# Performance work log

Hardware: AMD Instinct MI355X
Metric: run time of the kernel (lower is better)

## Reference

```python
import jax, jax.numpy as jnp
import numpy as np

DEPTH, HEADS, DIM_HEAD = 6, 12, 64
DIM, MLP, FEAT = 768, 3072, 1000
B, N = 32, 196
EPS = 1e-5


def layernorm(x, g, b):
    m = jnp.mean(x, axis=-1, keepdims=True)
    v = jnp.var(x, axis=-1, keepdims=True)
    return (x - m) * jax.lax.rsqrt(v + EPS) * g + b


def setup_inputs() -> dict:
    key = jax.random.key(0)
    ks = jax.random.split(key, 8)
    s = 0.02
    return {
        "x": jax.random.normal(ks[0], (B, N, DIM), jnp.float32),
        "cls_token": jax.random.normal(ks[1], (1, 1, DIM), jnp.float32),
        "ln1_g": jnp.ones((DEPTH, DIM), jnp.float32),
        "ln1_b": jnp.zeros((DEPTH, DIM), jnp.float32),
        "w_qkv": jax.random.normal(ks[2], (DEPTH, DIM, 3 * HEADS * DIM_HEAD), jnp.float32) * s,
        "reattn_w": jax.random.normal(ks[3], (DEPTH, HEADS, HEADS), jnp.float32),
        "reattn_g": jnp.ones((DEPTH, HEADS), jnp.float32),
        "reattn_b": jnp.zeros((DEPTH, HEADS), jnp.float32),
        "w_out": jax.random.normal(ks[4], (DEPTH, HEADS * DIM_HEAD, DIM), jnp.float32) * s,
        "b_out": jnp.zeros((DEPTH, DIM), jnp.float32),
        "ln2_g": jnp.ones((DEPTH, DIM), jnp.float32),
        "ln2_b": jnp.zeros((DEPTH, DIM), jnp.float32),
        "w1": jax.random.normal(ks[5], (DEPTH, DIM, MLP), jnp.float32) * s,
        "b1": jnp.zeros((DEPTH, MLP), jnp.float32),
        "w2": jax.random.normal(ks[6], (DEPTH, MLP, DIM), jnp.float32) * s,
        "b2": jnp.zeros((DEPTH, DIM), jnp.float32),
        "lnf_g": jnp.ones((DIM,), jnp.float32),
        "lnf_b": jnp.zeros((DIM,), jnp.float32),
        "w_head": jax.random.normal(ks[7], (DIM, FEAT), jnp.float32) * s,
        "b_head": jnp.zeros((FEAT,), jnp.float32),
    }


def _forward(x, cls_token, ln1_g, ln1_b, w_qkv, reattn_w, reattn_g, reattn_b,
             w_out, b_out, ln2_g, ln2_b, w1, b1, w2, b2, lnf_g, lnf_b, w_head, b_head):
    b = x.shape[0]
    cls = jnp.broadcast_to(cls_token, (b, 1, DIM))
    x = jnp.concatenate([cls, x], axis=1)  # (B, N+1, DIM)
    n = x.shape[1]
    scale = DIM_HEAD ** -0.5
    for l in range(DEPTH):
        h = layernorm(x, ln1_g[l], ln1_b[l])
        qkv = h @ w_qkv[l]                       # (B, n, 3*H*Dh)
        qkv = qkv.reshape(b, n, 3, HEADS, DIM_HEAD)
        q, k, v = (qkv[:, :, i].transpose(0, 2, 1, 3) for i in range(3))  # b h n d
        dots = jnp.einsum('bhid,bhjd->bhij', q, k) * scale
        attn = jax.nn.softmax(dots, axis=-1)
        attn = jnp.einsum('bhij,hg->bgij', attn, reattn_w[l])
        # per-head LayerNorm: normalize over head axis (axis=1)
        m = jnp.mean(attn, axis=1, keepdims=True)
        var = jnp.var(attn, axis=1, keepdims=True)
        attn = (attn - m) * jax.lax.rsqrt(var + EPS)
        attn = attn * reattn_g[l][None, :, None, None] + reattn_b[l][None, :, None, None]
        out = jnp.einsum('bhij,bhjd->bhid', attn, v)
        out = out.transpose(0, 2, 1, 3).reshape(b, n, HEADS * DIM_HEAD)
        x = x + out @ w_out[l] + b_out[l]
        h = layernorm(x, ln2_g[l], ln2_b[l])
        h = jax.nn.gelu(h @ w1[l] + b1[l], approximate=False)
        x = x + h @ w2[l] + b2[l]
    pooled = x[:, 0]  # cls pool
    return layernorm(pooled, lnf_g, lnf_b) @ w_head + b_head


def reference(x, cls_token, ln1_g, ln1_b, w_qkv, reattn_w, reattn_g, reattn_b,
              w_out, b_out, ln2_g, ln2_b, w1, b1, w2, b2, lnf_g, lnf_b, w_head, b_head):
    return _forward(x, cls_token, ln1_g, ln1_b, w_qkv, reattn_w, reattn_g, reattn_b,
                    w_out, b_out, ln2_g, ln2_b, w1, b1, w2, b2, lnf_g, lnf_b, w_head, b_head)
```

## Files before the change

kernel.cpp:

```cpp
#include <hip/hip_runtime.h>
#include <cstdint>

typedef __bf16 bf16_t;
typedef __bf16 bf16x8 __attribute__((ext_vector_type(8)));
typedef float  f32x4  __attribute__((ext_vector_type(4)));
typedef unsigned int u32;

#define DEPTH 6
#define HEADS 12
#define DH    64
#define DIM   768
#define MLPD  3072
#define FEAT  1000
#define BATCH 32
#define SEQ   197
#define NP    224
#define TOK   (BATCH*SEQ)

__device__ __forceinline__ f32x4 zero4() {
    f32x4 z; z[0] = 0.f; z[1] = 0.f; z[2] = 0.f; z[3] = 0.f; return z;
}

__device__ __forceinline__ f32x4 mfma16(bf16x8 a, bf16x8 b, f32x4 c) {
    return __builtin_amdgcn_mfma_f32_16x16x32_bf16(a, b, c, 0, 0, 0);
}

typedef const __attribute__((address_space(1))) u32* gas_ptr;
typedef __attribute__((address_space(3))) u32*       las_ptr;
__device__ __forceinline__ void gload16(const bf16_t* g, bf16_t* l) {
    __builtin_amdgcn_global_load_lds((gas_ptr)g, (las_ptr)l, 16, 0, 0);
}

__global__ __launch_bounds__(256) void concat_k(const float* __restrict__ x,
                                                const float* __restrict__ cls,
                                                float* __restrict__ xbuf) {
    int idx = blockIdx.x * 256 + threadIdx.x;
    int col = idx % DIM;
    int row = idx / DIM;
    int b = row / SEQ, p = row % SEQ;
    xbuf[idx] = (p == 0) ? cls[col] : x[(b * 196 + p - 1) * DIM + col];
}

__global__ __launch_bounds__(256) void tcvt_k(const float* __restrict__ W,
                                              bf16_t* __restrict__ Wt,
                                              int K, int N) {
    __shared__ float t[32][33];
    int n0 = blockIdx.x * 32, k0 = blockIdx.y * 32;
    int c = threadIdx.x & 31, r = threadIdx.x >> 5;
#pragma unroll
    for (int i = 0; i < 4; i++) {
        int k = k0 + r + i * 8, n = n0 + c;
        t[r + i * 8][c] = (n < N) ? W[k * N + n] : 0.f;
    }
    __syncthreads();
#pragma unroll
    for (int i = 0; i < 4; i++) {
        int n = n0 + r + i * 8, k = k0 + c;
        if (n < N) Wt[n * K + k] = (bf16_t)t[c][r + i * 8];
    }
}

__global__ __launch_bounds__(256) void tcvtall_k(const float* __restrict__ wq,
                                                 const float* __restrict__ wo,
                                                 const float* __restrict__ w1p,
                                                 const float* __restrict__ w2p,
                                                 bf16_t* __restrict__ wt) {
    int id = blockIdx.x;
    const float* W; int K, N, ntx, rid; long doff;
    if (id < 1728)      { W = wq;  K = 768;  N = 2304; doff = 0;       ntx = 72; rid = id; }
    else if (id < 2304) { W = wo;  K = 768;  N = 768;  doff = 1769472; ntx = 24; rid = id - 1728; }
    else if (id < 4608) { W = w1p; K = 768;  N = 3072; doff = 2359296; ntx = 96; rid = id - 2304; }
    else                { W = w2p; K = 3072; N = 768;  doff = 4718592; ntx = 24; rid = id - 4608; }
    int n0 = (rid % ntx) * 32, k0 = (rid / ntx) * 32;
    __shared__ float t[32][33];
    int c = threadIdx.x & 31, r = threadIdx.x >> 5;
#pragma unroll
    for (int i = 0; i < 4; i++)
        t[r + i * 8][c] = W[(long)(k0 + r + i * 8) * N + n0 + c];
    __syncthreads();
#pragma unroll
    for (int i = 0; i < 4; i++)
        wt[doff + (long)(n0 + r + i * 8) * K + k0 + c] = (bf16_t)t[c][r + i * 8];
}

__global__ __launch_bounds__(256) void ln_k(const float* __restrict__ x, long row_stride,
                                            const float* __restrict__ g,
                                            const float* __restrict__ b,
                                            bf16_t* __restrict__ out) {
    int row = blockIdx.x;
    const float* xr = x + (long)row * row_stride;
    int t = threadIdx.x;
    float v0 = xr[t], v1 = xr[t + 256], v2 = xr[t + 512];
    float s  = v0 + v1 + v2;
    float sq = v0 * v0 + v1 * v1 + v2 * v2;
#pragma unroll
    for (int o = 1; o < 64; o <<= 1) { s += __shfl_xor(s, o); sq += __shfl_xor(sq, o); }
    __shared__ float ss[4], sqs[4];
    int w = t >> 6;
    if ((t & 63) == 0) { ss[w] = s; sqs[w] = sq; }
    __syncthreads();
    s  = ss[0] + ss[1] + ss[2] + ss[3];
    sq = sqs[0] + sqs[1] + sqs[2] + sqs[3];
    float m  = s * (1.f / 768.f);
    float rs = rsqrtf(sq * (1.f / 768.f) - m * m + 1e-5f);
    bf16_t* orow = out + (long)row * DIM;
    orow[t]       = (bf16_t)((v0 - m) * rs * g[t]       + b[t]);
    orow[t + 256] = (bf16_t)((v1 - m) * rs * g[t + 256] + b[t + 256]);
    orow[t + 512] = (bf16_t)((v2 - m) * rs * g[t + 512] + b[t + 512]);
}

template <int MODE>
__global__ __launch_bounds__(512) void gemm_k(const bf16_t* __restrict__ A,
                                              const bf16_t* __restrict__ Bt,
                                              const float* __restrict__ bias,
                                              float* __restrict__ Cf,
                                              bf16_t* __restrict__ Cb,
                                              int M, int N, int Kstride, int Klen) {
    __shared__ bf16_t sA[2][128][32];
    __shared__ bf16_t sB[2][256][32];
    int tid = threadIdx.x;
    int bm = blockIdx.x * 128, bn = blockIdx.y * 256;
    long koff = (long)blockIdx.z * Klen;
    int wave = tid >> 6, lane = tid & 63;
    int wm = (wave >> 2) * 64, wn = (wave & 3) * 64;
    int la = lane & 15, lb = lane >> 4;

    int trow = tid >> 2, colE = (tid & 3) * 8;
    int rowA = bm + trow; if (rowA > M - 1) rowA = M - 1;
    int rowB0 = bn + trow, rowB1 = bn + 128 + trow;

    f32x4 acc[4][4];
#pragma unroll
    for (int m = 0; m < 4; m++)
#pragma unroll
        for (int n = 0; n < 4; n++) acc[m][n] = zero4();

    auto stage = [&](int buf, long k0) {
        gload16(A  + (long)rowA  * Kstride + k0 + colE, &sA[buf][0][0] + wave * 512);
        gload16(Bt + (long)rowB0 * Kstride + k0 + colE, &sB[buf][0][0] + wave * 512);
        gload16(Bt + (long)rowB1 * Kstride + k0 + colE, &sB[buf][0][0] + 4096 + wave * 512);
    };

    int nt = Klen >> 5;
    stage(0, koff);
    __syncthreads();
    for (int t = 0; t < nt; t++) {
        int cur = t & 1;
        if (t + 1 < nt) stage(cur ^ 1, koff + ((long)(t + 1) << 5));
        bf16x8 af[4], bfr[4];
#pragma unroll
        for (int m = 0; m < 4; m++) af[m]  = *(const bf16x8*)&sA[cur][wm + m * 16 + la][lb * 8];
#pragma unroll
        for (int n = 0; n < 4; n++) bfr[n] = *(const bf16x8*)&sB[cur][wn + n * 16 + la][lb * 8];
#pragma unroll
        for (int m = 0; m < 4; m++)
#pragma unroll
            for (int n = 0; n < 4; n++)
                acc[m][n] = mfma16(af[m], bfr[n], acc[m][n]);
        __syncthreads();
    }

    long kout = (long)blockIdx.z * M * (long)N;
#pragma unroll
    for (int m = 0; m < 4; m++) {
#pragma unroll
        for (int n = 0; n < 4; n++) {
            int ib = bm + wm + m * 16 + lb * 4;
            int jb = bn + wn + n * 16 + la;
            float bv = (MODE == 1 || MODE == 2) ? bias[jb] : 0.f;
#pragma unroll
            for (int r = 0; r < 4; r++) {
                int i = ib + r;
                if (i >= M) continue;
                float v = acc[m][n][r];
                if (MODE == 0) {
                    Cb[(long)i * N + jb] = (bf16_t)v;
                } else if (MODE == 1) {
                    Cf[(long)i * N + jb] += v + bv;
                } else if (MODE == 2) {
                    float u = v + bv;
                    Cb[(long)i * N + jb] = (bf16_t)(0.5f * u * (1.f + erff(u * 0.70710678118f)));
                } else {
                    Cf[kout + (long)i * N + jb] = v;
                }
            }
        }
    }
}

__global__ __launch_bounds__(256) void redk_k(float* __restrict__ xbuf,
                                              const float* __restrict__ part,
                                              const float* __restrict__ bias) {
    const long total = (long)TOK * DIM;
    for (long idx = blockIdx.x * 256 + threadIdx.x; idx < total; idx += (long)gridDim.x * 256) {
        int col = (int)(idx % DIM);
        xbuf[idx] += part[idx] + part[idx + total] + bias[col];
    }
}

__global__ __launch_bounds__(256) void gemm_h(const bf16_t* __restrict__ A,
                                              const bf16_t* __restrict__ Bt,
                                              const float* __restrict__ bias,
                                              float* __restrict__ Cf,
                                              int M, int N, int K) {
    __shared__ bf16_t sA[2][128][32];
    __shared__ bf16_t sB[2][128][32];
    int tid = threadIdx.x;
    int bm = blockIdx.x * 128, bn = blockIdx.y * 128;
    int wave = tid >> 6, lane = tid & 63;
    int wm = (wave >> 1) * 64, wn = (wave & 1) * 64;
    int la = lane & 15, lb = lane >> 4;
    int rowA[2], rowB[2], colE[2];
#pragma unroll
    for (int q = 0; q < 2; q++) {
        int li = (wave * 2 + q) * 64 + lane;
        int row = li >> 2;
        colE[q] = (li & 3) * 8;
        int ar = bm + row; if (ar > M - 1) ar = M - 1;
        int br = bn + row; if (br > N - 1) br = N - 1;
        rowA[q] = ar; rowB[q] = br;
    }
    f32x4 acc[4][4];
#pragma unroll
    for (int m = 0; m < 4; m++)
#pragma unroll
        for (int n = 0; n < 4; n++) acc[m][n] = zero4();
    int nt = K >> 5;
#pragma unroll
    for (int q = 0; q < 2; q++) {
        gload16(A  + (long)rowA[q] * K + colE[q], &sA[0][0][0] + (wave * 2 + q) * 512);
        gload16(Bt + (long)rowB[q] * K + colE[q], &sB[0][0][0] + (wave * 2 + q) * 512);
    }
    __syncthreads();
    for (int t = 0; t < nt; t++) {
        int cur = t & 1;
        if (t + 1 < nt) {
            int k0 = (t + 1) << 5;
#pragma unroll
            for (int q = 0; q < 2; q++) {
                gload16(A  + (long)rowA[q] * K + k0 + colE[q], &sA[cur ^ 1][0][0] + (wave * 2 + q) * 512);
                gload16(Bt + (long)rowB[q] * K + k0 + colE[q], &sB[cur ^ 1][0][0] + (wave * 2 + q) * 512);
            }
        }
        bf16x8 af[4], bfr[4];
#pragma unroll
        for (int m = 0; m < 4; m++) af[m]  = *(const bf16x8*)&sA[cur][wm + m * 16 + la][lb * 8];
#pragma unroll
        for (int n = 0; n < 4; n++) bfr[n] = *(const bf16x8*)&sB[cur][wn + n * 16 + la][lb * 8];
#pragma unroll
        for (int m = 0; m < 4; m++)
#pragma unroll
            for (int n = 0; n < 4; n++)
                acc[m][n] = mfma16(af[m], bfr[n], acc[m][n]);
        __syncthreads();
    }
#pragma unroll
    for (int m = 0; m < 4; m++) {
#pragma unroll
        for (int n = 0; n < 4; n++) {
            int ib = bm + wm + m * 16 + lb * 4;
            int jb = bn + wn + n * 16 + la;
            if (jb >= N) continue;
            float bv = bias[jb];
#pragma unroll
            for (int r = 0; r < 4; r++) {
                int i = ib + r;
                if (i >= M) continue;
                Cf[(long)i * N + jb] = acc[m][n][r] + bv;
            }
        }
    }
}

__global__ __launch_bounds__(256) void qk_k(const bf16_t* __restrict__ qkv,
                                            float* __restrict__ dots) {
    int bh = blockIdx.z;
    int b = bh / HEADS, h = bh % HEADS;
    int i0 = blockIdx.x * 64, j0 = blockIdx.y * 64;
    __shared__ bf16_t sQ[64][32], sK[64][32];
    int tid = threadIdx.x, wave = tid >> 6, lane = tid & 63;
    int wm = (wave >> 1) * 32, wn = (wave & 1) * 32;
    int la = lane & 15, lb = lane >> 4;
    f32x4 acc[2][2];
#pragma unroll
    for (int m = 0; m < 2; m++)
#pragma unroll
        for (int n = 0; n < 2; n++) acc[m][n] = zero4();

    int row = tid >> 2, col = (tid & 3) * 8;
    int qi = i0 + row; if (qi > SEQ - 1) qi = SEQ - 1;
    int kj = j0 + row; if (kj > SEQ - 1) kj = SEQ - 1;
    const bf16_t* qsrc = qkv + (((b * SEQ + qi) * 3 + 0) * HEADS + h) * DH + col;
    const bf16_t* ksrc = qkv + (((b * SEQ + kj) * 3 + 1) * HEADS + h) * DH + col;

#pragma unroll
    for (int d0 = 0; d0 < 64; d0 += 32) {
        *(bf16x8*)&sQ[row][col] = *(const bf16x8*)(qsrc + d0);
        *(bf16x8*)&sK[row][col] = *(const bf16x8*)(ksrc + d0);
        __syncthreads();
        bf16x8 af[2], bfr[2];
#pragma unroll
        for (int m = 0; m < 2; m++) af[m]  = *(const bf16x8*)&sQ[wm + m * 16 + la][lb * 8];
#pragma unroll
        for (int n = 0; n < 2; n++) bfr[n] = *(const bf16x8*)&sK[wn + n * 16 + la][lb * 8];
#pragma unroll
        for (int m = 0; m < 2; m++)
#pragma unroll
            for (int n = 0; n < 2; n++)
                acc[m][n] = mfma16(af[m], bfr[n], acc[m][n]);
        __syncthreads();
    }
#pragma unroll
    for (int m = 0; m < 2; m++)
#pragma unroll
        for (int n = 0; n < 2; n++)
#pragma unroll
            for (int r = 0; r < 4; r++) {
                int i = i0 + wm + m * 16 + lb * 4 + r;
                int j = j0 + wn + n * 16 + la;
                if (i < SEQ && j < SEQ)
                    dots[((long)bh * SEQ + i) * NP + j] = acc[m][n][r] * 0.125f;
            }
}

__global__ __launch_bounds__(256) void smre_k(const float* __restrict__ dots,
                                              const float* __restrict__ W,
                                              const float* __restrict__ gg,
                                              const float* __restrict__ bb,
                                              bf16_t* __restrict__ attn2) {
    __shared__ float sm[HEADS][NP];
    __shared__ float sW[HEADS * HEADS];
    __shared__ float sg[HEADS], sb[HEADS];
    int tid = threadIdx.x;
    if (tid < HEADS * HEADS) sW[tid] = W[tid];
    if (tid < HEADS) { sg[tid] = gg[tid]; sb[tid] = bb[tid]; }
    int bi = blockIdx.x;
    int b = bi / SEQ, i = bi % SEQ;
    int wave = tid >> 6, lane = tid & 63;

    for (int h = wave; h < HEADS; h += 4) {
        const float* p = dots + ((long)(b * HEADS + h) * SEQ + i) * NP;
        float v[4], e[4];
#pragma unroll
        for (int q = 0; q < 4; q++) { int j = lane + 64 * q; v[q] = (j < SEQ) ? p[j] : -3.0e38f; }
        float mx = fmaxf(fmaxf(v[0], v[1]), fmaxf(v[2], v[3]));
#pragma unroll
        for (int o = 1; o < 64; o <<= 1) mx = fmaxf(mx, __shfl_xor(mx, o));
        float s = 0.f;
#pragma unroll
        for (int q = 0; q < 4; q++) {
            int j = lane + 64 * q;
            e[q] = (j < SEQ) ? __expf(v[q] - mx) : 0.f;
            s += e[q];
        }
#pragma unroll
        for (int o = 1; o < 64; o <<= 1) s += __shfl_xor(s, o);
        float inv = 1.f / s;
#pragma unroll
        for (int q = 0; q < 4; q++) { int j = lane + 64 * q; if (j < NP) sm[h][j] = e[q] * inv; }
    }
    __syncthreads();

    int j = tid;
    if (j >= NP) return;
    bool valid = j < SEQ;
    float vals[HEADS];
#pragma unroll
    for (int h = 0; h < HEADS; h++) vals[h] = valid ? sm[h][j] : 0.f;
    float mix[HEADS];
    float s = 0.f, sq = 0.f;
#pragma unroll
    for (int g = 0; g < HEADS; g++) {
        float a = 0.f;
#pragma unroll
        for (int h = 0; h < HEADS; h++) a += vals[h] * sW[h * HEADS + g];
        mix[g] = a; s += a; sq += a * a;
    }
    float m  = s * (1.f / 12.f);
    float rs = rsqrtf(sq * (1.f / 12.f) - m * m + 1e-5f);
    long base = ((long)(b * HEADS) * SEQ + i) * NP + j;
    const long hs = (long)SEQ * NP;
#pragma unroll
    for (int g = 0; g < HEADS; g++) {
        float o = valid ? ((mix[g] - m) * rs * sg[g] + sb[g]) : 0.f;
        attn2[base + g * hs] = (bf16_t)o;
    }
}

__global__ __launch_bounds__(256) void pv_k(const bf16_t* __restrict__ attn2,
                                            const bf16_t* __restrict__ qkv,
                                            bf16_t* __restrict__ aout) {
    int bh = blockIdx.y;
    int b = bh / HEADS, h = bh % HEADS;
    int i0 = blockIdx.x * 64;
    __shared__ bf16_t sP[64][32];
    __shared__ bf16_t sVt[64][32];
    int tid = threadIdx.x, wave = tid >> 6, lane = tid & 63;
    int wm = (wave >> 1) * 32, wn = (wave & 1) * 32;
    int la = lane & 15, lb = lane >> 4;
    f32x4 acc[2][2];
#pragma unroll
    for (int m = 0; m < 2; m++)
#pragma unroll
        for (int n = 0; n < 2; n++) acc[m][n] = zero4();

    int prow = tid >> 2, pcol = (tid & 3) * 8;
    int pi = i0 + prow; if (pi > SEQ - 1) pi = SEQ - 1;
    const bf16_t* psrc = attn2 + ((long)bh * SEQ + pi) * NP + pcol;
    int jl = tid >> 3, dblk = (tid & 7) * 8;
    int jlx = jl ^ ((tid & 3) << 3);

    for (int j0 = 0; j0 < NP; j0 += 32) {
        *(bf16x8*)&sP[prow][pcol] = *(const bf16x8*)(psrc + j0);
        int jg = j0 + jl;
        bf16x8 vv;
#pragma unroll
        for (int e = 0; e < 8; e++) vv[e] = (bf16_t)0.f;
        if (jg < SEQ)
            vv = *(const bf16x8*)(qkv + (((b * SEQ + jg) * 3 + 2) * HEADS + h) * DH + dblk);
#pragma unroll
        for (int e = 0; e < 8; e++) sVt[dblk + e][jlx] = vv[e];
        __syncthreads();
        bf16x8 af[2], bfr[2];
#pragma unroll
        for (int m = 0; m < 2; m++) af[m] = *(const bf16x8*)&sP[wm + m * 16 + la][lb * 8];
#pragma unroll
        for (int n = 0; n < 2; n++) {
            int rowd = wn + n * 16 + la;
            int colj = (lb * 8) ^ (((rowd >> 3) & 3) << 3);
            bfr[n] = *(const bf16x8*)&sVt[rowd][colj];
        }
#pragma unroll
        for (int m = 0; m < 2; m++)
#pragma unroll
            for (int n = 0; n < 2; n++)
                acc[m][n] = mfma16(af[m], bfr[n], acc[m][n]);
        __syncthreads();
    }
#pragma unroll
    for (int m = 0; m < 2; m++)
#pragma unroll
        for (int n = 0; n < 2; n++)
#pragma unroll
            for (int r = 0; r < 4; r++) {
                int i = i0 + wm + m * 16 + lb * 4 + r;
                int d = wn + n * 16 + la;
                if (i < SEQ)
                    aout[((long)b * SEQ + i) * DIM + h * DH + d] = (bf16_t)acc[m][n][r];
            }
}

extern "C" void kernel_launch(void* const* d_in, const int* in_sizes, int n_in,
                              void* d_out, int out_size, void* d_ws, size_t ws_size,
                              hipStream_t stream) {
    const float* x        = (const float*)d_in[0];
    const float* cls      = (const float*)d_in[1];
    const float* ln1_g    = (const float*)d_in[2];
    const float* ln1_b    = (const float*)d_in[3];
    const float* w_qkv    = (const float*)d_in[4];
    const float* reattn_w = (const float*)d_in[5];
    const float* reattn_g = (const float*)d_in[6];
    const float* reattn_b = (const float*)d_in[7];
    const float* w_out    = (const float*)d_in[8];
    const float* b_out    = (const float*)d_in[9];
    const float* ln2_g    = (const float*)d_in[10];
    const float* ln2_b    = (const float*)d_in[11];
    const float* w1       = (const float*)d_in[12];
    const float* b1       = (const float*)d_in[13];
    const float* w2       = (const float*)d_in[14];
    const float* b2       = (const float*)d_in[15];
    const float* lnf_g    = (const float*)d_in[16];
    const float* lnf_b    = (const float*)d_in[17];
    const float* w_head   = (const float*)d_in[18];
    const float* b_head   = (const float*)d_in[19];
    float* out = (float*)d_out;

    char* p = (char*)d_ws;
    auto alloc = [&](size_t bytes) -> char* {
        char* r = p;
        p += (bytes + 255) & ~(size_t)255;
        return r;
    };
    bf16_t* wt      = (bf16_t*)alloc(2ULL * 7077888);
    bf16_t* wt_head = (bf16_t*)alloc(2ULL * FEAT * DIM);
    float*  xbuf    = (float*)alloc(4ULL * TOK * DIM);
    bf16_t* h_ln    = (bf16_t*)alloc(2ULL * TOK * DIM);
    bf16_t* qkv     = (bf16_t*)alloc(2ULL * TOK * 3 * DIM);
    float*  dots    = (float*)alloc(4ULL * BATCH * HEADS * SEQ * NP);
    bf16_t* h_mid   = (bf16_t*)dots;
    bf16_t* attn2   = (bf16_t*)alloc(2ULL * BATCH * HEADS * SEQ * NP);
    bf16_t* aout    = (bf16_t*)alloc(2ULL * TOK * DIM);
    float*  part_op = (float*)dots;
    float*  part_m2 = (float*)attn2;

    dim3 B256(256), B512(512);
    concat_k<<<(TOK * DIM) / 256, B256, 0, stream>>>(x, cls, xbuf);
    tcvt_k<<<dim3((FEAT + 31) / 32, DIM / 32), B256, 0, stream>>>(w_head, wt_head, DIM, FEAT);

    bf16_t* wqkv_t = wt;
    bf16_t* wout_t = wt + 1769472;
    bf16_t* w1_t   = wt + 2359296;
    bf16_t* w2_t   = wt + 4718592;

    for (int l = 0; l < DEPTH; l++) {
        tcvtall_k<<<6912, B256, 0, stream>>>(w_qkv + (long)l * DIM * 2304,
                                             w_out + (long)l * DIM * DIM,
                                             w1 + (long)l * DIM * MLPD,
                                             w2 + (long)l * MLPD * DIM, wt);
        ln_k<<<TOK, B256, 0, stream>>>(xbuf, DIM, ln1_g + l * DIM, ln1_b + l * DIM, h_ln);
        gemm_k<0><<<dim3(50, 9), B512, 0, stream>>>(h_ln, wqkv_t, nullptr, nullptr, qkv, TOK, 2304, DIM, DIM);
        qk_k<<<dim3(4, 4, BATCH * HEADS), B256, 0, stream>>>(qkv, dots);
        smre_k<<<TOK, B256, 0, stream>>>(
            dots, reattn_w + l * HEADS * HEADS, reattn_g + l * HEADS, reattn_b + l * HEADS, attn2);
        pv_k<<<dim3(4, BATCH * HEADS), B256, 0, stream>>>(attn2, qkv, aout);
        gemm_k<3><<<dim3(50, 3, 2), B512, 0, stream>>>(aout, wout_t, nullptr, part_op, nullptr,
                                                       TOK, DIM, DIM, DIM / 2);
        redk_k<<<2048, B256, 0, stream>>>(xbuf, part_op, b_out + l * DIM);
        ln_k<<<TOK, B256, 0, stream>>>(xbuf, DIM, ln2_g + l * DIM, ln2_b + l * DIM, h_ln);
        gemm_k<2><<<dim3(50, 12), B512, 0, stream>>>(h_ln, w1_t, b1 + l * MLPD, nullptr, h_mid, TOK, MLPD, DIM, DIM);
        gemm_k<3><<<dim3(50, 3, 2), B512, 0, stream>>>(h_mid, w2_t, nullptr, part_m2, nullptr,
                                                       TOK, DIM, MLPD, MLPD / 2);
        redk_k<<<2048, B256, 0, stream>>>(xbuf, part_m2, b2 + l * DIM);
    }

    ln_k<<<BATCH, B256, 0, stream>>>(xbuf, (long)SEQ * DIM, lnf_g, lnf_b, h_ln);
    gemm_h<<<dim3(1, 8), B256, 0, stream>>>(h_ln, wt_head, b_head, out, BATCH, FEAT, DIM);
}
```

Before: 1.795 ms.

## Fuse split-K reduction with layernorm, store dots as bf16, use 4-way split-K

Replaces the grid-stride split-K reduction kernel with a per-row kernel that adds the partial sums and bias into the residual and applies the next layernorm in the same pass. This removes the separate ln_k launches and one extra read of xbuf. The QK scores are now stored in bf16 instead of fp32, which halves dots traffic at some cost in precision. The MLP down-projection uses 4-way split-K for more parallelism, which needs a larger partial buffer and a reshuffled workspace layout. The variance is computed as E[x^2]-m^2 in one pass, which is less numerically stable.

```diff
diff --git a/kernel.cpp b/kernel.cpp
--- a/kernel.cpp
+++ b/kernel.cpp
@@ -188,13 +188,45 @@
     }
 }
 
-__global__ __launch_bounds__(256) void redk_k(float* __restrict__ xbuf,
-                                              const float* __restrict__ part,
-                                              const float* __restrict__ bias) {
+template <int NC, bool DOLN>
+__global__ __launch_bounds__(256) void redln_k(float* __restrict__ xbuf,
+                                               const float* __restrict__ part,
+                                               const float* __restrict__ bias,
+                                               const float* __restrict__ g,
+                                               const float* __restrict__ b,
+                                               bf16_t* __restrict__ out) {
+    int row = blockIdx.x, t = threadIdx.x;
+    long base = (long)row * DIM;
     const long total = (long)TOK * DIM;
-    for (long idx = blockIdx.x * 256 + threadIdx.x; idx < total; idx += (long)gridDim.x * 256) {
-        int col = (int)(idx % DIM);
-        xbuf[idx] += part[idx] + part[idx + total] + bias[col];
+    float v[3];
+    float s = 0.f, sq = 0.f;
+#pragma unroll
+    for (int q = 0; q < 3; q++) {
+        int col = t + q * 256;
+        long idx = base + col;
+        float val = xbuf[idx] + bias[col];
+#pragma unroll
+        for (int k = 0; k < NC; k++) val += part[idx + (long)k * total];
+        xbuf[idx] = val;
+        v[q] = val; s += val; sq += val * val;
+    }
+    if (DOLN) {
+#pragma unroll
+        for (int o = 1; o < 64; o <<= 1) { s += __shfl_xor(s, o); sq += __shfl_xor(sq, o); }
+        __shared__ float ss[4], sqs[4];
+        int w = t >> 6;
+        if ((t & 63) == 0) { ss[w] = s; sqs[w] = sq; }
+        __syncthreads();
+        s  = ss[0] + ss[1] + ss[2] + ss[3];
+        sq = sqs[0] + sqs[1] + sqs[2] + sqs[3];
+        float m  = s * (1.f / 768.f);
+        float rs = rsqrtf(sq * (1.f / 768.f) - m * m + 1e-5f);
+        bf16_t* orow = out + base;
+#pragma unroll
+        for (int q = 0; q < 3; q++) {
+            int col = t + q * 256;
+            orow[col] = (bf16_t)((v[q] - m) * rs * g[col] + b[col]);
+        }
     }
 }
 
@@ -273,7 +305,7 @@
 }
 
 __global__ __launch_bounds__(256) void qk_k(const bf16_t* __restrict__ qkv,
-                                            float* __restrict__ dots) {
+                                            bf16_t* __restrict__ dots) {
     int bh = blockIdx.z;
     int b = bh / HEADS, h = bh % HEADS;
     int i0 = blockIdx.x * 64, j0 = blockIdx.y * 64;
@@ -319,11 +351,11 @@
                 int i = i0 + wm + m * 16 + lb * 4 + r;
                 int j = j0 + wn + n * 16 + la;
                 if (i < SEQ && j < SEQ)
-                    dots[((long)bh * SEQ + i) * NP + j] = acc[m][n][r] * 0.125f;
+                    dots[((long)bh * SEQ + i) * NP + j] = (bf16_t)(acc[m][n][r] * 0.125f);
             }
 }
 
-__global__ __launch_bounds__(256) void smre_k(const float* __restrict__ dots,
+__global__ __launch_bounds__(256) void smre_k(const bf16_t* __restrict__ dots,
                                               const float* __restrict__ W,
                                               const float* __restrict__ gg,
                                               const float* __restrict__ bb,
@@ -339,10 +371,10 @@
     int wave = tid >> 6, lane = tid & 63;
 
     for (int h = wave; h < HEADS; h += 4) {
-        const float* p = dots + ((long)(b * HEADS + h) * SEQ + i) * NP;
+        const bf16_t* p = dots + ((long)(b * HEADS + h) * SEQ + i) * NP;
         float v[4], e[4];
 #pragma unroll
-        for (int q = 0; q < 4; q++) { int j = lane + 64 * q; v[q] = (j < SEQ) ? p[j] : -3.0e38f; }
+        for (int q = 0; q < 4; q++) { int j = lane + 64 * q; v[q] = (j < SEQ) ? (float)p[j] : -3.0e38f; }
         float mx = fmaxf(fmaxf(v[0], v[1]), fmaxf(v[2], v[3]));
 #pragma unroll
         for (int o = 1; o < 64; o <<= 1) mx = fmaxf(mx, __shfl_xor(mx, o));
@@ -486,11 +518,13 @@
     float*  xbuf    = (float*)alloc(4ULL * TOK * DIM);
     bf16_t* h_ln    = (bf16_t*)alloc(2ULL * TOK * DIM);
     bf16_t* qkv     = (bf16_t*)alloc(2ULL * TOK * 3 * DIM);
-    float*  dots    = (float*)alloc(4ULL * BATCH * HEADS * SEQ * NP);
-    bf16_t* h_mid   = (bf16_t*)dots;
+    char*   dreg    = alloc(2ULL * TOK * MLPD);
+    bf16_t* dots    = (bf16_t*)dreg;
+    bf16_t* h_mid   = (bf16_t*)dreg;
+    float*  part_op = (float*)dreg;
     bf16_t* attn2   = (bf16_t*)alloc(2ULL * BATCH * HEADS * SEQ * NP);
     bf16_t* aout    = (bf16_t*)alloc(2ULL * TOK * DIM);
-    float*  part_op = (float*)dots;
+    alloc(4ULL * 4 * TOK * DIM - 2ULL * BATCH * HEADS * SEQ * NP - 2ULL * TOK * DIM);
     float*  part_m2 = (float*)attn2;
 
     dim3 B256(256), B512(512);
@@ -501,13 +535,14 @@
     bf16_t* wout_t = wt + 1769472;
     bf16_t* w1_t   = wt + 2359296;
     bf16_t* w2_t   = wt + 4718592;
+
+    ln_k<<<TOK, B256, 0, stream>>>(xbuf, DIM, ln1_g, ln1_b, h_ln);
 
     for (int l = 0; l < DEPTH; l++) {
         tcvtall_k<<<6912, B256, 0, stream>>>(w_qkv + (long)l * DIM * 2304,
                                              w_out + (long)l * DIM * DIM,
                                              w1 + (long)l * DIM * MLPD,
                                              w2 + (long)l * MLPD * DIM, wt);
-        ln_k<<<TOK, B256, 0, stream>>>(xbuf, DIM, ln1_g + l * DIM, ln1_b + l * DIM, h_ln);
         gemm_k<0><<<dim3(50, 9), B512, 0, stream>>>(h_ln, wqkv_t, nullptr, nullptr, qkv, TOK, 2304, DIM, DIM);
         qk_k<<<dim3(4, 4, BATCH * HEADS), B256, 0, stream>>>(qkv, dots);
         smre_k<<<TOK, B256, 0, stream>>>(
@@ -515,12 +550,17 @@
         pv_k<<<dim3(4, BATCH * HEADS), B256, 0, stream>>>(attn2, qkv, aout);
         gemm_k<3><<<dim3(50, 3, 2), B512, 0, stream>>>(aout, wout_t, nullptr, part_op, nullptr,
                                                        TOK, DIM, DIM, DIM / 2);
-        redk_k<<<2048, B256, 0, stream>>>(xbuf, part_op, b_out + l * DIM);
-        ln_k<<<TOK, B256, 0, stream>>>(xbuf, DIM, ln2_g + l * DIM, ln2_b + l * DIM, h_ln);
+        redln_k<2, true><<<TOK, B256, 0, stream>>>(xbuf, part_op, b_out + l * DIM,
+                                                   ln2_g + l * DIM, ln2_b + l * DIM, h_ln);
         gemm_k<2><<<dim3(50, 12), B512, 0, stream>>>(h_ln, w1_t, b1 + l * MLPD, nullptr, h_mid, TOK, MLPD, DIM, DIM);
-        gemm_k<3><<<dim3(50, 3, 2), B512, 0, stream>>>(h_mid, w2_t, nullptr, part_m2, nullptr,
-                                                       TOK, DIM, MLPD, MLPD / 2);
-        redk_k<<<2048, B256, 0, stream>>>(xbuf, part_m2, b2 + l * DIM);
+        gemm_k<3><<<dim3(50, 3, 4), B512, 0, stream>>>(h_mid, w2_t, nullptr, part_m2, nullptr,
+                                                       TOK, DIM, MLPD, MLPD / 4);
+        if (l < DEPTH - 1)
+            redln_k<4, true><<<TOK, B256, 0, stream>>>(xbuf, part_m2, b2 + l * DIM,
+                                                       ln1_g + (l + 1) * DIM, ln1_b + (l + 1) * DIM, h_ln);
+        else
+            redln_k<4, false><<<TOK, B256, 0, stream>>>(xbuf, part_m2, b2 + l * DIM,
+                                                        nullptr, nullptr, nullptr);
     }
 
     ln_k<<<BATCH, B256, 0, stream>>>(xbuf, (long)SEQ * DIM, lnf_g, lnf_b, h_ln);
```

Result: faster. 1.751 ms (median of 2 runs) (-2.5%).
